# Kernel tuning notes

Hardware: AMD Instinct MI355X
Metric: run time of the kernel (lower is better)

Reference implementation:

```python
import jax, jax.numpy as jnp
import numpy as np

B, D_IN, D_OUT, N_SUBNET, G = 16384, 512, 512, 8, 2


def setup_inputs() -> dict:
    key = jax.random.key(0)
    k_x, k_g, k_w = jax.random.split(key, 3)
    x = jax.random.normal(k_x, (B, D_IN), dtype=jnp.float32)
    groups = jax.random.randint(k_g, (B, G), 0, N_SUBNET, dtype=jnp.int32)
    # per-expert Dense params (the 'subnets')
    W = jax.random.normal(k_w, (N_SUBNET, D_IN, D_OUT), dtype=jnp.float32) * (1.0 / np.sqrt(D_IN))
    b = jnp.zeros((N_SUBNET, D_OUT), dtype=jnp.float32)
    return {"x": x, "groups": groups, "W": W, "b": b}


def reference(x, groups, W, b):
    """SubnetGate: one-hot gated dispatch to per-group subnets + combine.

    Faithful math: gates = one_hot(groups[:, group_col], n_subnet);
    out = sum_e gates[:, e] * subnet_e(x). Since gates are one-hot the
    combine selects exactly one expert output per row (gate weight 1.0).
    """
    group_col = 0
    n_subnet = W.shape[0]
    idx_group = groups[:, group_col]                     # [B]
    gates = jax.nn.one_hot(idx_group, n_subnet, dtype=x.dtype)  # [B, E]
    # run every expert on the full batch (dense reference for the
    # gather-compute-scatter kernel), then gate-combine
    expert_out = jnp.einsum("bi,eio->beo", x, W) + b[None, :, :]  # [B, E, O]
    out = jnp.einsum("be,beo->bo", gates, expert_out)             # [B, O]
    return out
```

## Files before the change

### kernel.cpp

```cpp
#include <hip/hip_runtime.h>
#include <hip/hip_bf16.h>


#define NROWS   16384
#define KDIM    512
#define NDIM    512
#define NEXP    8
#define MAX_DESC 264
#define WS_NDESC_OFF   64
#define WS_DESC_OFF    128
#define WS_ROWLIST_OFF 4096
#define WS_WT_OFF      (4096 + NEXP * NROWS * 4)
#define WS_XG_OFF      (WS_WT_OFF + NEXP * KDIM * NDIM * 2)
#define WS_NEED        ((size_t)WS_XG_OFF + (size_t)MAX_DESC * 8 * 4096 * 2)

typedef __bf16        bf16x8 __attribute__((ext_vector_type(8)));
typedef float         f32x4  __attribute__((ext_vector_type(4)));
typedef unsigned int  u32x4  __attribute__((ext_vector_type(4)));

__device__ __forceinline__ unsigned int f2bf_u(float f) {
    unsigned int u = __builtin_bit_cast(unsigned int, f);
    return (u + 0x7FFFu + ((u >> 16) & 1u)) >> 16;
}
__device__ __forceinline__ unsigned int pack2(float a, float b) {
    return f2bf_u(a) | (f2bf_u(b) << 16);
}
__device__ __forceinline__ u32x4 pack8(f32x4 a, f32x4 b) {
    u32x4 p;
    p.x = pack2(a.x, a.y); p.y = pack2(a.z, a.w);
    p.z = pack2(b.x, b.y); p.w = pack2(b.z, b.w);
    return p;
}

__global__ void zero_kernel(int* __restrict__ gcnt) {
    if (threadIdx.x < NEXP) gcnt[threadIdx.x] = 0;
}

__global__ void hist_kernel(const int* __restrict__ groups,
                            int* __restrict__ gcnt,
                            int* __restrict__ rowlist) {
    __shared__ int lcnt[NEXP];
    __shared__ int lbase[NEXP];
    const int tid = threadIdx.x;
    const int base = blockIdx.x * 256;
    if (tid < NEXP) lcnt[tid] = 0;
    __syncthreads();
    int r = base + tid;
    int e = groups[r * 2];
    int pos = atomicAdd(&lcnt[e], 1);
    __syncthreads();
    if (tid < NEXP) lbase[tid] = atomicAdd(&gcnt[tid], lcnt[tid]);
    __syncthreads();
    rowlist[e * NROWS + lbase[e] + pos] = r;
}

__global__ void plan_kernel(const int* __restrict__ counts,
                            int* __restrict__ ndesc,
                            int* __restrict__ desc) {
    if (threadIdx.x == 0) {
        int M = 0;
        for (int e = 0; e < NEXP; ++e) {
            int nmt = (counts[e] + 63) >> 6;
            for (int mt = 0; mt < nmt && M < MAX_DESC; ++mt)
                desc[M++] = (e << 16) | mt;
        }
        ndesc[0] = M;
    }
}

__global__ __launch_bounds__(256, 4)
void stage_kernel(const float* __restrict__ x,
                  const float* __restrict__ W,
                  const int* __restrict__ counts,
                  const int* __restrict__ rowlist,
                  const int* __restrict__ ndesc,
                  const int* __restrict__ desc,
                  unsigned short* __restrict__ Wf,
                  unsigned short* __restrict__ xf) {
    const int bid = blockIdx.x;
    const int tid = threadIdx.x;

    if (bid < 64) {
        const int e  = bid >> 3;
        const int kt = bid & 7;
        const float* Wb = W + (size_t)e * (KDIM * NDIM);
        unsigned short* dst = Wf + ((size_t)(e * 8 + kt)) * 32768;
        #pragma unroll
        for (int it = 0; it < 16; ++it) {
            int gidx = it * 256 + tid;
            int lane = gidx & 63;
            int nf   = (gidx >> 6) & 31;
            int kf   = gidx >> 11;
            int q    = lane >> 4;
            int l15  = lane & 15;
            int n    = nf * 16 + l15;
            int k0   = kt * 64 + kf * 32 + q * 8;
            unsigned int p[4];
            #pragma unroll
            for (int jj = 0; jj < 4; ++jj)
                p[jj] = pack2(Wb[(size_t)(k0 + 2 * jj) * NDIM + n],
                              Wb[(size_t)(k0 + 2 * jj + 1) * NDIM + n]);
            *(u32x4*)&dst[(size_t)gidx * 8] = *(const u32x4*)p;
        }
    } else {
        const int b2 = bid - 64;
        const int d  = b2 >> 3;
        const int kt = b2 & 7;
        if (d >= ndesc[0]) return;
        const int de = desc[d];
        const int e  = de >> 16;
        const int mt = de & 0xffff;
        int m_valid = counts[e] - mt * 64;
        if (m_valid > 64) m_valid = 64;
        const int* rl = rowlist + e * NROWS + mt * 64;
        unsigned short* dst = xf + ((size_t)(d * 8 + kt)) * 4096;
        #pragma unroll
        for (int it = 0; it < 2; ++it) {
            int gidx = it * 256 + tid;
            int lane = gidx & 63;
            int mf   = (gidx >> 6) & 3;
            int kf   = gidx >> 8;
            int q    = lane >> 4;
            int l15  = lane & 15;
            int m    = mf * 16 + l15;
            u32x4 p = {0u, 0u, 0u, 0u};
            if (m < m_valid) {
                const float* s = x + (size_t)rl[m] * KDIM + kt * 64 + kf * 32 + q * 8;
                p = pack8(*(const f32x4*)s, *(const f32x4*)(s + 4));
            }
            *(u32x4*)&dst[(size_t)gidx * 8] = p;
        }
    }
}

__global__ __launch_bounds__(256, 3)
void gemm_frag(const unsigned short* __restrict__ xf,
               const int* __restrict__ counts,
               const int* __restrict__ rowlist,
               const unsigned short* __restrict__ Wf,
               const float* __restrict__ bias,
               float* __restrict__ out,
               const int* __restrict__ ndesc,
               const int* __restrict__ desc) {
    const int tid = threadIdx.x;
    const int w   = tid >> 6;
    const int ln  = tid & 63;
    const int q   = ln >> 4;
    const int l15 = ln & 15;

    const int Twaves = ndesc[0] * 16;
    for (int wt = blockIdx.x * 4 + w; wt < Twaves; wt += gridDim.x * 4) {
        const int d     = wt >> 4;
        const int half  = (wt >> 3) & 1;
        const int strip = wt & 7;
        const int de = desc[d];
        const int e  = de >> 16;
        const int mt = de & 0xffff;
        int m_valid = counts[e] - mt * 64;
        if (m_valid > 64) m_valid = 64;
        const int* rl = rowlist + e * NROWS + mt * 64;

        const unsigned short* ab = xf + (size_t)d * 32768 + (half * 2) * 512 + ln * 8;
        const unsigned short* bb = Wf + (size_t)e * 262144 + (strip * 4) * 512 + ln * 8;

        f32x4 acc[2][4];
        #pragma unroll
        for (int mi = 0; mi < 2; ++mi)
            #pragma unroll
            for (int ni = 0; ni < 4; ++ni)
                acc[mi][ni] = (f32x4){0.f, 0.f, 0.f, 0.f};

        bf16x8 af[2][2], bv[2][4];
        #pragma unroll
        for (int mi = 0; mi < 2; ++mi)
            af[0][mi] = *(const bf16x8*)(ab + mi * 512);
        #pragma unroll
        for (int ni = 0; ni < 4; ++ni)
            bv[0][ni] = *(const bf16x8*)(bb + ni * 512);

        #pragma unroll
        for (int s = 0; s < 16; ++s) {
            const int buf = s & 1;
            if (s < 15) {
                const int s1 = s + 1;
                const int kt = s1 >> 1, kf = s1 & 1;
                const unsigned short* a1 = ab + kt * 4096 + kf * 2048;
                const unsigned short* b1 = bb + kt * 32768 + kf * 16384;
                #pragma unroll
                for (int mi = 0; mi < 2; ++mi)
                    af[buf ^ 1][mi] = *(const bf16x8*)(a1 + mi * 512);
                #pragma unroll
                for (int ni = 0; ni < 4; ++ni)
                    bv[buf ^ 1][ni] = *(const bf16x8*)(b1 + ni * 512);
            }
            #pragma unroll
            for (int mi = 0; mi < 2; ++mi)
                #pragma unroll
                for (int ni = 0; ni < 4; ++ni)
                    acc[mi][ni] = __builtin_amdgcn_mfma_f32_16x16x32_bf16(
                        af[buf][mi], bv[buf][ni], acc[mi][ni], 0, 0, 0);
        }

        int growv[8];
        #pragma unroll
        for (int mi = 0; mi < 2; ++mi)
            #pragma unroll
            for (int r = 0; r < 4; ++r) {
                int rloc = half * 32 + mi * 16 + q * 4 + r;
                growv[mi * 4 + r] = (rloc < m_valid) ? rl[rloc] : -1;
            }
        #pragma unroll
        for (int ni = 0; ni < 4; ++ni) {
            int col = strip * 64 + ni * 16 + l15;
            float bvs = bias[e * NDIM + col];
            #pragma unroll
            for (int mi = 0; mi < 2; ++mi)
                #pragma unroll
                for (int r = 0; r < 4; ++r) {
                    int gr = growv[mi * 4 + r];
                    if (gr >= 0) out[(size_t)gr * NDIM + col] = acc[mi][ni][r] + bvs;
                }
        }
    }
}

extern "C" void kernel_launch(void* const* d_in, const int* in_sizes, int n_in,
                              void* d_out, int out_size, void* d_ws, size_t ws_size,
                              hipStream_t stream) {
    const float* x      = (const float*)d_in[0];
    const int*   groups = (const int*)d_in[1];
    const float* W      = (const float*)d_in[2];
    const float* b      = (const float*)d_in[3];
    float*       out    = (float*)d_out;

    char* ws = (char*)d_ws;
    int*            counts  = (int*)ws;
    int*            ndesc   = (int*)(ws + WS_NDESC_OFF);
    int*            desc    = (int*)(ws + WS_DESC_OFF);
    int*            rowlist = (int*)(ws + WS_ROWLIST_OFF);
    unsigned short* Wf      = (unsigned short*)(ws + WS_WT_OFF);
    unsigned short* xf      = (unsigned short*)(ws + WS_XG_OFF);

    zero_kernel<<<1, 64, 0, stream>>>(counts);
    hist_kernel<<<64, 256, 0, stream>>>(groups, counts, rowlist);
    plan_kernel<<<1, 64, 0, stream>>>(counts, ndesc, desc);
    stage_kernel<<<64 + MAX_DESC * 8, 256, 0, stream>>>(x, W, counts, rowlist,
                                                        ndesc, desc, Wf, xf);
    gemm_frag<<<1056, 256, 0, stream>>>(xf, counts, rowlist, Wf, b, out,
                                        ndesc, desc);
}
```

Measured before the change: 132.6 us.

## Enlarge per-wave GEMM tile to 64x64 with triple-buffered fragment loads

Each wave now computes a full 64-row by 64-column tile instead of a 32x64 half, which doubles A-fragment reuse across the B loads. The grid-stride loop over wave tiles is replaced by a fixed 576-block grid that maps blockIdx to a column strip and a group of descriptors. Register prefetch goes from double to triple buffering. Occupancy drops from 3 to 2 blocks per SIMD to fit the extra registers. The zero kernel is also replaced with hipMemsetAsync.

```diff
diff --git a/kernel.cpp b/kernel.cpp
--- a/kernel.cpp
+++ b/kernel.cpp
@@ -12,7 +12,6 @@
 #define WS_ROWLIST_OFF 4096
 #define WS_WT_OFF      (4096 + NEXP * NROWS * 4)
 #define WS_XG_OFF      (WS_WT_OFF + NEXP * KDIM * NDIM * 2)
-#define WS_NEED        ((size_t)WS_XG_OFF + (size_t)MAX_DESC * 8 * 4096 * 2)
 
 typedef __bf16        bf16x8 __attribute__((ext_vector_type(8)));
 typedef float         f32x4  __attribute__((ext_vector_type(4)));
@@ -30,10 +29,6 @@
     p.x = pack2(a.x, a.y); p.y = pack2(a.z, a.w);
     p.z = pack2(b.x, b.y); p.w = pack2(b.z, b.w);
     return p;
-}
-
-__global__ void zero_kernel(int* __restrict__ gcnt) {
-    if (threadIdx.x < NEXP) gcnt[threadIdx.x] = 0;
 }
 
 __global__ void hist_kernel(const int* __restrict__ groups,
@@ -133,7 +128,7 @@
     }
 }
 
-__global__ __launch_bounds__(256, 3)
+__global__ __launch_bounds__(256, 2)
 void gemm_frag(const unsigned short* __restrict__ xf,
                const int* __restrict__ counts,
                const int* __restrict__ rowlist,
@@ -148,79 +143,92 @@
     const int q   = ln >> 4;
     const int l15 = ln & 15;
 
-    const int Twaves = ndesc[0] * 16;
-    for (int wt = blockIdx.x * 4 + w; wt < Twaves; wt += gridDim.x * 4) {
-        const int d     = wt >> 4;
-        const int half  = (wt >> 3) & 1;
-        const int strip = wt & 7;
-        const int de = desc[d];
-        const int e  = de >> 16;
-        const int mt = de & 0xffff;
-        int m_valid = counts[e] - mt * 64;
-        if (m_valid > 64) m_valid = 64;
-        const int* rl = rowlist + e * NROWS + mt * 64;
-
-        const unsigned short* ab = xf + (size_t)d * 32768 + (half * 2) * 512 + ln * 8;
-        const unsigned short* bb = Wf + (size_t)e * 262144 + (strip * 4) * 512 + ln * 8;
-
-        f32x4 acc[2][4];
-        #pragma unroll
-        for (int mi = 0; mi < 2; ++mi)
+    const int nd  = ndesc[0];
+    const int nd4 = (nd + 3) >> 2;
+    const int Gj  = (nd4 + 7) >> 3;
+
+    const int j     = blockIdx.x & 7;
+    const int i     = blockIdx.x >> 3;
+    const int strip = i / 9;
+    const int gl    = i - strip * 9;
+    if (gl >= Gj) return;
+    const int g = j * Gj + gl;
+    if (g >= nd4) return;
+    const int d = g * 4 + w;
+    if (d >= nd) return;
+
+    const int de = desc[d];
+    const int e  = de >> 16;
+    const int mt = de & 0xffff;
+    int m_valid = counts[e] - mt * 64;
+    if (m_valid > 64) m_valid = 64;
+    const int* rl = rowlist + e * NROWS + mt * 64;
+
+    const unsigned short* ab = xf + (size_t)d * 32768 + ln * 8;
+    const unsigned short* bb = Wf + (size_t)e * 262144 + strip * 4 * 512 + ln * 8;
+
+    f32x4 acc[4][4];
+    #pragma unroll
+    for (int mi = 0; mi < 4; ++mi)
+        #pragma unroll
+        for (int ni = 0; ni < 4; ++ni)
+            acc[mi][ni] = (f32x4){0.f, 0.f, 0.f, 0.f};
+
+    bf16x8 af[3][4], bv[3][4];
+    #pragma unroll
+    for (int s = 0; s < 2; ++s) {
+        const int ao = (s >> 1) * 4096 + (s & 1) * 2048;
+        const int bo = (s >> 1) * 32768 + (s & 1) * 16384;
+        #pragma unroll
+        for (int mi = 0; mi < 4; ++mi)
+            af[s][mi] = *(const bf16x8*)(ab + ao + mi * 512);
+        #pragma unroll
+        for (int ni = 0; ni < 4; ++ni)
+            bv[s][ni] = *(const bf16x8*)(bb + bo + ni * 512);
+    }
+
+    #pragma unroll
+    for (int s = 0; s < 16; ++s) {
+        const int cur = s % 3;
+        if (s + 2 < 16) {
+            const int s2  = s + 2;
+            const int nxt = s2 % 3;
+            const int ao = (s2 >> 1) * 4096 + (s2 & 1) * 2048;
+            const int bo = (s2 >> 1) * 32768 + (s2 & 1) * 16384;
+            #pragma unroll
+            for (int mi = 0; mi < 4; ++mi)
+                af[nxt][mi] = *(const bf16x8*)(ab + ao + mi * 512);
             #pragma unroll
             for (int ni = 0; ni < 4; ++ni)
-                acc[mi][ni] = (f32x4){0.f, 0.f, 0.f, 0.f};
-
-        bf16x8 af[2][2], bv[2][4];
-        #pragma unroll
-        for (int mi = 0; mi < 2; ++mi)
-            af[0][mi] = *(const bf16x8*)(ab + mi * 512);
-        #pragma unroll
-        for (int ni = 0; ni < 4; ++ni)
-            bv[0][ni] = *(const bf16x8*)(bb + ni * 512);
-
-        #pragma unroll
-        for (int s = 0; s < 16; ++s) {
-            const int buf = s & 1;
-            if (s < 15) {
-                const int s1 = s + 1;
-                const int kt = s1 >> 1, kf = s1 & 1;
-                const unsigned short* a1 = ab + kt * 4096 + kf * 2048;
-                const unsigned short* b1 = bb + kt * 32768 + kf * 16384;
-                #pragma unroll
-                for (int mi = 0; mi < 2; ++mi)
-                    af[buf ^ 1][mi] = *(const bf16x8*)(a1 + mi * 512);
-                #pragma unroll
-                for (int ni = 0; ni < 4; ++ni)
-                    bv[buf ^ 1][ni] = *(const bf16x8*)(b1 + ni * 512);
+                bv[nxt][ni] = *(const bf16x8*)(bb + bo + ni * 512);
+        }
+        #pragma unroll
+        for (int mi = 0; mi < 4; ++mi)
+            #pragma unroll
+            for (int ni = 0; ni < 4; ++ni)
+                acc[mi][ni] = __builtin_amdgcn_mfma_f32_16x16x32_bf16(
+                    af[cur][mi], bv[cur][ni], acc[mi][ni], 0, 0, 0);
+    }
+
+    int growv[16];
+    #pragma unroll
+    for (int mi = 0; mi < 4; ++mi)
+        #pragma unroll
+        for (int r = 0; r < 4; ++r) {
+            int rloc = mi * 16 + q * 4 + r;
+            growv[mi * 4 + r] = (rloc < m_valid) ? rl[rloc] : -1;
+        }
+    #pragma unroll
+    for (int ni = 0; ni < 4; ++ni) {
+        int col = strip * 64 + ni * 16 + l15;
+        float bvs = bias[e * NDIM + col];
+        #pragma unroll
+        for (int mi = 0; mi < 4; ++mi)
+            #pragma unroll
+            for (int r = 0; r < 4; ++r) {
+                int gr = growv[mi * 4 + r];
+                if (gr >= 0) out[(size_t)gr * NDIM + col] = acc[mi][ni][r] + bvs;
             }
-            #pragma unroll
-            for (int mi = 0; mi < 2; ++mi)
-                #pragma unroll
-                for (int ni = 0; ni < 4; ++ni)
-                    acc[mi][ni] = __builtin_amdgcn_mfma_f32_16x16x32_bf16(
-                        af[buf][mi], bv[buf][ni], acc[mi][ni], 0, 0, 0);
-        }
-
-        int growv[8];
-        #pragma unroll
-        for (int mi = 0; mi < 2; ++mi)
-            #pragma unroll
-            for (int r = 0; r < 4; ++r) {
-                int rloc = half * 32 + mi * 16 + q * 4 + r;
-                growv[mi * 4 + r] = (rloc < m_valid) ? rl[rloc] : -1;
-            }
-        #pragma unroll
-        for (int ni = 0; ni < 4; ++ni) {
-            int col = strip * 64 + ni * 16 + l15;
-            float bvs = bias[e * NDIM + col];
-            #pragma unroll
-            for (int mi = 0; mi < 2; ++mi)
-                #pragma unroll
-                for (int r = 0; r < 4; ++r) {
-                    int gr = growv[mi * 4 + r];
-                    if (gr >= 0) out[(size_t)gr * NDIM + col] = acc[mi][ni][r] + bvs;
-                }
-        }
     }
 }
 
@@ -241,11 +249,11 @@
     unsigned short* Wf      = (unsigned short*)(ws + WS_WT_OFF);
     unsigned short* xf      = (unsigned short*)(ws + WS_XG_OFF);
 
-    zero_kernel<<<1, 64, 0, stream>>>(counts);
+    hipMemsetAsync(counts, 0, NEXP * sizeof(int), stream);
     hist_kernel<<<64, 256, 0, stream>>>(groups, counts, rowlist);
     plan_kernel<<<1, 64, 0, stream>>>(counts, ndesc, desc);
     stage_kernel<<<64 + MAX_DESC * 8, 256, 0, stream>>>(x, W, counts, rowlist,
                                                         ndesc, desc, Wf, xf);
-    gemm_frag<<<1056, 256, 0, stream>>>(xf, counts, rowlist, Wf, b, out,
-                                        ndesc, desc);
-}
+    gemm_frag<<<576, 256, 0, stream>>>(xf, counts, rowlist, Wf, b, out,
+                                       ndesc, desc);
+}
```

After: 131.7 us. Within noise of the previous version (-0.7%).
